# Kernel optimization log

Hardware: AMD Instinct MI355X
Metric: run time of the kernel (lower is better)

Reference implementation:

```python
import jax, jax.numpy as jnp
import numpy as np


def setup_inputs() -> dict:
    key = jax.random.key(0)
    k1, k2, k3, k4, k5 = jax.random.split(key, 5)
    F_total, T, D, K = 256, 576, 1408, 144  # frames, in_token_num, num_features, out_token_num
    return {
        "image_embeds": jax.random.normal(k1, (F_total, T, D), jnp.float32),
        "pre_w": jax.random.normal(k2, (1, D), jnp.float32) * 0.02,
        "pre_b": jax.random.normal(k3, (1,), jnp.float32) * 0.02,
        "trans_weight": jax.random.normal(k4, (T, T), jnp.float32) * 0.02,
        "trans_bias": jax.random.normal(k5, (T,), jnp.float32) * 0.02,
        "n_frames": 32,
        "out_token_num": K,
    }


def reference(image_embeds, pre_w, pre_b, trans_weight, trans_bias, n_frames, out_token_num):
    # image_embeds: [F_total, T, D]
    F_total, T, D = image_embeds.shape
    # pre_proj: Linear(D, 1) -> per-token scalar score, [F_total, T]
    s = jnp.einsum('ftd,d->ft', image_embeds, pre_w[0]) + pre_b[0]
    # [F,1,T] @ [T,T] + bias -> squeeze(1) == [F,T] @ W + b
    logits = s @ trans_weight + trans_bias                    # [F_total, T]
    scores = jax.nn.softmax(logits, axis=-1)                  # [F_total, T]
    # top-k via descending argsort, then restore ascending token order
    idx = jnp.sort(jnp.argsort(-scores, axis=-1)[:, :out_token_num], axis=-1)  # [F_total, K]
    sel = jnp.take_along_axis(image_embeds, idx[:, :, None], axis=1)           # [F_total, K, D]
    # torch returns a list of per-video tensors; with uniform n_frames this is
    # equivalently a stacked [n_videos, n_frames, K, D] array.
    n_videos = F_total // n_frames
    return sel.reshape(n_videos, n_frames, out_token_num, D)
```

## Files before the change

kernel.cpp:

```cpp
#include <hip/hip_runtime.h>
#include <stdint.h>

typedef float f4 __attribute__((ext_vector_type(4)));

__device__ __forceinline__ double dot4d(f4 a, f4 b) {
    return (double)a.x * (double)b.x + (double)a.y * (double)b.y
         + (double)a.z * (double)b.z + (double)a.w * (double)b.w;
}

template <int T, int D, int K>
__global__ __launch_bounds__(1024)
void fused_opt_kernel(const float* __restrict__ x,
                      const float* __restrict__ pre_w,
                      const float* __restrict__ pre_b,
                      const float* __restrict__ W,
                      const float* __restrict__ bias,
                      float* __restrict__ out) {
    constexpr int N4 = D / 4;
    constexpr int NJ = N4 / 8;
    constexpr int NG = 128;
    constexpr int NW = (T + 31) / 32;

    __shared__ f4       w_sh[N4];
    __shared__ double   s_sh[T];
    __shared__ double   lg[T];
    __shared__ unsigned flags[NW];
    __shared__ int      sel[K];

    const int f   = blockIdx.x;
    const int tid = threadIdx.x;
    const int sub = tid & 7;
    const int gid = tid >> 3;

    for (int i = tid; i < N4; i += 1024) w_sh[i] = ((const f4*)pre_w)[i];
    if (tid < NW) flags[tid] = 0u;
    __syncthreads();

    const double pb = (double)pre_b[0];
    for (int r = gid; r < T; r += NG) {
        const f4* xr = (const f4*)(x + ((size_t)f * T + r) * D);
        double a0 = 0, a1 = 0, a2 = 0, a3 = 0;
        #pragma unroll 2
        for (int j = 0; j < NJ; j += 4) {
            f4 v0 = xr[sub + 8 * (j + 0)];
            f4 v1 = xr[sub + 8 * (j + 1)];
            f4 v2 = xr[sub + 8 * (j + 2)];
            f4 v3 = xr[sub + 8 * (j + 3)];
            f4 u0 = w_sh[sub + 8 * (j + 0)];
            f4 u1 = w_sh[sub + 8 * (j + 1)];
            f4 u2 = w_sh[sub + 8 * (j + 2)];
            f4 u3 = w_sh[sub + 8 * (j + 3)];
            a0 += dot4d(v0, u0);
            a1 += dot4d(v1, u1);
            a2 += dot4d(v2, u2);
            a3 += dot4d(v3, u3);
        }
        double a = (a0 + a1) + (a2 + a3);
        a += __shfl_down(a, 4, 8);
        a += __shfl_down(a, 2, 8);
        a += __shfl_down(a, 1, 8);
        if (sub == 0) s_sh[r] = a + pb;
    }
    __syncthreads();

    if (tid < T) {
        const float* Wc = W + tid;
        double acc[8] = {0, 0, 0, 0, 0, 0, 0, 0};
        for (int tp = 0; tp < T; tp += 8) {
            #pragma unroll
            for (int u = 0; u < 8; ++u)
                acc[u] += s_sh[tp + u] * (double)Wc[(size_t)(tp + u) * T];
        }
        double r01 = (acc[0] + acc[1]) + (acc[2] + acc[3]);
        double r23 = (acc[4] + acc[5]) + (acc[6] + acc[7]);
        lg[tid] = (r01 + r23) + (double)bias[tid];
    }
    __syncthreads();

    if (tid < T) {
        const double v = lg[tid];
        int rank = 0;
        #pragma unroll 8
        for (int tp = 0; tp < T; ++tp) {
            double u = lg[tp];
            rank += (u > v) || (u == v && tp < tid);
        }
        if (rank < K) atomicOr(&flags[tid >> 5], 1u << (tid & 31));
    }
    __syncthreads();

    if (tid < T) {
        if ((flags[tid >> 5] >> (tid & 31)) & 1u) {
            int pos = __popc(flags[tid >> 5] & ((1u << (tid & 31)) - 1u));
            for (int u2 = 0; u2 < (tid >> 5); ++u2) pos += __popc(flags[u2]);
            sel[pos] = tid;
        }
    }
    __syncthreads();

    for (int k2 = gid; k2 < K; k2 += NG) {
        const int t = sel[k2];
        const f4* src = (const f4*)(x + ((size_t)f * T + t) * D);
        f4*       dst = (f4*)(out + ((size_t)f * K + k2) * D);
        #pragma unroll 2
        for (int j = 0; j < NJ; j += 4) {
            f4 v0 = src[sub + 8 * (j + 0)];
            f4 v1 = src[sub + 8 * (j + 1)];
            f4 v2 = src[sub + 8 * (j + 2)];
            f4 v3 = src[sub + 8 * (j + 3)];
            __builtin_nontemporal_store(v0, &dst[sub + 8 * (j + 0)]);
            __builtin_nontemporal_store(v1, &dst[sub + 8 * (j + 1)]);
            __builtin_nontemporal_store(v2, &dst[sub + 8 * (j + 2)]);
            __builtin_nontemporal_store(v3, &dst[sub + 8 * (j + 3)]);
        }
    }
}

__global__ __launch_bounds__(1024)
void fused_select_kernel(const float* __restrict__ x,
                         const float* __restrict__ pre_w,
                         const float* __restrict__ pre_b,
                         const float* __restrict__ W,
                         const float* __restrict__ bias,
                         float* __restrict__ out,
                         int T, int D, int K) {
    __shared__ double   s_sh[1024];
    __shared__ double   lg[1024];
    __shared__ unsigned flags[32];
    __shared__ int      sel[576];

    const int f    = blockIdx.x;
    const int tid  = threadIdx.x;
    const int wave = tid >> 6;
    const int lane = tid & 63;
    const int nw   = blockDim.x >> 6;
    const int n4   = D >> 2;

    const f4* wv = (const f4*)pre_w;
    for (int t = wave; t < T; t += nw) {
        const f4* xr = (const f4*)(x + ((size_t)f * T + t) * D);
        double acc = 0.0;
        for (int p = lane; p < n4; p += 64) {
            f4 a = xr[p], c = wv[p];
            acc += dot4d(a, c);
        }
#pragma unroll
        for (int off = 32; off > 0; off >>= 1) acc += __shfl_down(acc, off);
        if (lane == 0) s_sh[t] = acc + (double)pre_b[0];
    }
    if (tid < 32) flags[tid] = 0u;
    __syncthreads();

    if (tid < T) {
        const float* Wc = W + tid;
        double a0 = 0, a1 = 0, a2 = 0, a3 = 0;
        int tp = 0;
        for (; tp + 4 <= T; tp += 4) {
            a0 += s_sh[tp + 0] * (double)Wc[(size_t)(tp + 0) * T];
            a1 += s_sh[tp + 1] * (double)Wc[(size_t)(tp + 1) * T];
            a2 += s_sh[tp + 2] * (double)Wc[(size_t)(tp + 2) * T];
            a3 += s_sh[tp + 3] * (double)Wc[(size_t)(tp + 3) * T];
        }
        for (; tp < T; ++tp) a0 += s_sh[tp] * (double)Wc[(size_t)tp * T];
        lg[tid] = ((a0 + a1) + (a2 + a3)) + (double)bias[tid];
    }
    __syncthreads();
    if (tid < T) {
        const double v = lg[tid];
        int rank = 0;
        for (int tp = 0; tp < T; ++tp) {
            double u = lg[tp];
            rank += (u > v) || (u == v && tp < tid);
        }
        if (rank < K) atomicOr(&flags[tid >> 5], 1u << (tid & 31));
    }
    __syncthreads();
    if (tid < T) {
        if ((flags[tid >> 5] >> (tid & 31)) & 1u) {
            int pos = __popc(flags[tid >> 5] & ((1u << (tid & 31)) - 1u));
            for (int u2 = 0; u2 < (tid >> 5); ++u2) pos += __popc(flags[u2]);
            sel[pos] = tid;
        }
    }
    __syncthreads();
    for (int k2 = wave; k2 < K; k2 += nw) {
        int t = sel[k2];
        const f4* src = (const f4*)(x + ((size_t)f * T + t) * D);
        f4*       dst = (f4*)(out + ((size_t)f * K + k2) * D);
        for (int p = lane; p < n4; p += 64)
            __builtin_nontemporal_store(src[p], &dst[p]);
    }
}

extern "C" void kernel_launch(void* const* d_in, const int* in_sizes, int n_in,
                              void* d_out, int out_size, void* d_ws, size_t ws_size,
                              hipStream_t stream) {
    const float* x     = (const float*)d_in[0];
    const float* pre_w = (const float*)d_in[1];
    const float* pre_b = (const float*)d_in[2];
    const float* W     = (const float*)d_in[3];
    const float* bias  = (const float*)d_in[4];
    float* outp = (float*)d_out;

    const int D = in_sizes[1];
    const int T = in_sizes[4];
    const int F = in_sizes[0] / (T * D);
    const int K = out_size / (F * D);

    if (T == 576 && D == 1408 && K == 144) {
        fused_opt_kernel<576, 1408, 144><<<F, 1024, 0, stream>>>(
            x, pre_w, pre_b, W, bias, outp);
    } else {
        fused_select_kernel<<<F, 1024, 0, stream>>>(x, pre_w, pre_b, W, bias,
                                                    outp, T, D, K);
    }
}
```

Before: 263.1 us.

## Split fused per-frame kernel into score, select and gather kernels

Replaces the single per-frame fused kernel with three launches: a grid-wide row-dot score kernel writing scores to workspace, a per-frame select kernel computing logits and top-k indices, and a grid-wide gather kernel copying selected rows. This aims to spread the bandwidth-bound streaming phases across many small blocks instead of one large block per frame, so serial select work no longer stalls memory streaming. It adds workspace traffic, extra launches, and loses any cache reuse of x between scoring and gathering.

```diff
diff --git a/kernel.cpp b/kernel.cpp
--- a/kernel.cpp
+++ b/kernel.cpp
@@ -8,62 +8,69 @@
          + (double)a.z * (double)b.z + (double)a.w * (double)b.w;
 }
 
-template <int T, int D, int K>
-__global__ __launch_bounds__(1024)
-void fused_opt_kernel(const float* __restrict__ x,
-                      const float* __restrict__ pre_w,
-                      const float* __restrict__ pre_b,
-                      const float* __restrict__ W,
-                      const float* __restrict__ bias,
-                      float* __restrict__ out) {
+template <int T, int D>
+__global__ __launch_bounds__(256)
+void score_kernel(const float* __restrict__ x,
+                  const float* __restrict__ pre_w,
+                  const float* __restrict__ pre_b,
+                  double* __restrict__ s,
+                  int nrows) {
     constexpr int N4 = D / 4;
     constexpr int NJ = N4 / 8;
-    constexpr int NG = 128;
+
+    __shared__ f4 w_sh[N4];
+
+    const int tid = threadIdx.x;
+    const int sub = tid & 7;
+    const int row = (blockIdx.x * 256 + tid) >> 3;
+
+    for (int i = tid; i < N4; i += 256) w_sh[i] = ((const f4*)pre_w)[i];
+    __syncthreads();
+    if (row >= nrows) return;
+
+    const f4* xr = (const f4*)(x + (size_t)row * D);
+    double a0 = 0, a1 = 0, a2 = 0, a3 = 0;
+    #pragma unroll 2
+    for (int j = 0; j < NJ; j += 4) {
+        f4 v0 = xr[sub + 8 * (j + 0)];
+        f4 v1 = xr[sub + 8 * (j + 1)];
+        f4 v2 = xr[sub + 8 * (j + 2)];
+        f4 v3 = xr[sub + 8 * (j + 3)];
+        f4 u0 = w_sh[sub + 8 * (j + 0)];
+        f4 u1 = w_sh[sub + 8 * (j + 1)];
+        f4 u2 = w_sh[sub + 8 * (j + 2)];
+        f4 u3 = w_sh[sub + 8 * (j + 3)];
+        a0 += dot4d(v0, u0);
+        a1 += dot4d(v1, u1);
+        a2 += dot4d(v2, u2);
+        a3 += dot4d(v3, u3);
+    }
+    double a = (a0 + a1) + (a2 + a3);
+    a += __shfl_down(a, 4, 8);
+    a += __shfl_down(a, 2, 8);
+    a += __shfl_down(a, 1, 8);
+    if (sub == 0) s[row] = a + (double)pre_b[0];
+}
+
+template <int T, int K>
+__global__ __launch_bounds__(T)
+void select_kernel(const double* __restrict__ s,
+                   const float* __restrict__ W,
+                   const float* __restrict__ bias,
+                   int* __restrict__ idx_out) {
     constexpr int NW = (T + 31) / 32;
-
-    __shared__ f4       w_sh[N4];
     __shared__ double   s_sh[T];
     __shared__ double   lg[T];
     __shared__ unsigned flags[NW];
-    __shared__ int      sel[K];
 
     const int f   = blockIdx.x;
     const int tid = threadIdx.x;
-    const int sub = tid & 7;
-    const int gid = tid >> 3;
-
-    for (int i = tid; i < N4; i += 1024) w_sh[i] = ((const f4*)pre_w)[i];
+
+    s_sh[tid] = s[(size_t)f * T + tid];
     if (tid < NW) flags[tid] = 0u;
     __syncthreads();
 
-    const double pb = (double)pre_b[0];
-    for (int r = gid; r < T; r += NG) {
-        const f4* xr = (const f4*)(x + ((size_t)f * T + r) * D);
-        double a0 = 0, a1 = 0, a2 = 0, a3 = 0;
-        #pragma unroll 2
-        for (int j = 0; j < NJ; j += 4) {
-            f4 v0 = xr[sub + 8 * (j + 0)];
-            f4 v1 = xr[sub + 8 * (j + 1)];
-            f4 v2 = xr[sub + 8 * (j + 2)];
-            f4 v3 = xr[sub + 8 * (j + 3)];
-            f4 u0 = w_sh[sub + 8 * (j + 0)];
-            f4 u1 = w_sh[sub + 8 * (j + 1)];
-            f4 u2 = w_sh[sub + 8 * (j + 2)];
-            f4 u3 = w_sh[sub + 8 * (j + 3)];
-            a0 += dot4d(v0, u0);
-            a1 += dot4d(v1, u1);
-            a2 += dot4d(v2, u2);
-            a3 += dot4d(v3, u3);
-        }
-        double a = (a0 + a1) + (a2 + a3);
-        a += __shfl_down(a, 4, 8);
-        a += __shfl_down(a, 2, 8);
-        a += __shfl_down(a, 1, 8);
-        if (sub == 0) s_sh[r] = a + pb;
-    }
-    __syncthreads();
-
-    if (tid < T) {
+    {
         const float* Wc = W + tid;
         double acc[8] = {0, 0, 0, 0, 0, 0, 0, 0};
         for (int tp = 0; tp < T; tp += 8) {
@@ -77,7 +84,7 @@
     }
     __syncthreads();
 
-    if (tid < T) {
+    {
         const double v = lg[tid];
         int rank = 0;
         #pragma unroll 8
@@ -89,30 +96,44 @@
     }
     __syncthreads();
 
-    if (tid < T) {
+    {
         if ((flags[tid >> 5] >> (tid & 31)) & 1u) {
             int pos = __popc(flags[tid >> 5] & ((1u << (tid & 31)) - 1u));
             for (int u2 = 0; u2 < (tid >> 5); ++u2) pos += __popc(flags[u2]);
-            sel[pos] = tid;
-        }
-    }
-    __syncthreads();
-
-    for (int k2 = gid; k2 < K; k2 += NG) {
-        const int t = sel[k2];
-        const f4* src = (const f4*)(x + ((size_t)f * T + t) * D);
-        f4*       dst = (f4*)(out + ((size_t)f * K + k2) * D);
-        #pragma unroll 2
-        for (int j = 0; j < NJ; j += 4) {
-            f4 v0 = src[sub + 8 * (j + 0)];
-            f4 v1 = src[sub + 8 * (j + 1)];
-            f4 v2 = src[sub + 8 * (j + 2)];
-            f4 v3 = src[sub + 8 * (j + 3)];
-            __builtin_nontemporal_store(v0, &dst[sub + 8 * (j + 0)]);
-            __builtin_nontemporal_store(v1, &dst[sub + 8 * (j + 1)]);
-            __builtin_nontemporal_store(v2, &dst[sub + 8 * (j + 2)]);
-            __builtin_nontemporal_store(v3, &dst[sub + 8 * (j + 3)]);
-        }
+            idx_out[(size_t)f * K + pos] = tid;
+        }
+    }
+}
+
+template <int T, int D, int K>
+__global__ __launch_bounds__(256)
+void gather_kernel(const float* __restrict__ x,
+                   const int* __restrict__ idx,
+                   float* __restrict__ out,
+                   int nrows) {
+    constexpr int N4 = D / 4;
+    constexpr int NJ = N4 / 8;
+
+    const int tid = threadIdx.x;
+    const int sub = tid & 7;
+    const int row = (blockIdx.x * 256 + tid) >> 3;
+    if (row >= nrows) return;
+
+    const int f = row / K;
+    const int t = idx[row];
+
+    const f4* src = (const f4*)(x + ((size_t)f * T + t) * D);
+    f4*       dst = (f4*)(out + (size_t)row * D);
+    #pragma unroll 2
+    for (int j = 0; j < NJ; j += 4) {
+        f4 v0 = src[sub + 8 * (j + 0)];
+        f4 v1 = src[sub + 8 * (j + 1)];
+        f4 v2 = src[sub + 8 * (j + 2)];
+        f4 v3 = src[sub + 8 * (j + 3)];
+        __builtin_nontemporal_store(v0, &dst[sub + 8 * (j + 0)]);
+        __builtin_nontemporal_store(v1, &dst[sub + 8 * (j + 1)]);
+        __builtin_nontemporal_store(v2, &dst[sub + 8 * (j + 2)]);
+        __builtin_nontemporal_store(v3, &dst[sub + 8 * (j + 3)]);
     }
 }
 
@@ -140,10 +161,7 @@
     for (int t = wave; t < T; t += nw) {
         const f4* xr = (const f4*)(x + ((size_t)f * T + t) * D);
         double acc = 0.0;
-        for (int p = lane; p < n4; p += 64) {
-            f4 a = xr[p], c = wv[p];
-            acc += dot4d(a, c);
-        }
+        for (int p = lane; p < n4; p += 64) acc += dot4d(xr[p], wv[p]);
 #pragma unroll
         for (int off = 32; off > 0; off >>= 1) acc += __shfl_down(acc, off);
         if (lane == 0) s_sh[t] = acc + (double)pre_b[0];
@@ -208,8 +226,18 @@
     const int K = out_size / (F * D);
 
     if (T == 576 && D == 1408 && K == 144) {
-        fused_opt_kernel<576, 1408, 144><<<F, 1024, 0, stream>>>(
-            x, pre_w, pre_b, W, bias, outp);
+        double* s_buf = (double*)d_ws;
+        int*    idx   = (int*)((char*)d_ws + (size_t)F * T * sizeof(double));
+
+        const int nrows1 = F * T;
+        score_kernel<576, 1408><<<(nrows1 * 8 + 255) / 256, 256, 0, stream>>>(
+            x, pre_w, pre_b, s_buf, nrows1);
+
+        select_kernel<576, 144><<<F, 576, 0, stream>>>(s_buf, W, bias, idx);
+
+        const int nrows3 = F * K;
+        gather_kernel<576, 1408, 144><<<(nrows3 * 8 + 255) / 256, 256, 0, stream>>>(
+            x, idx, outp, nrows3);
     } else {
         fused_select_kernel<<<F, 1024, 0, stream>>>(x, pre_w, pre_b, W, bias,
                                                     outp, T, D, K);
```

After: 283.0 us. 7.6% more time.
